# Kernel optimization log

Hardware: AMD Instinct MI355X
Metric: run time of the kernel (lower is better)

Reference implementation:

```python
import jax, jax.numpy as jnp
import numpy as np

# Module config (from init_kwargs)
B = 1024          # batch
CIN = 1024        # in_channels
COUT = 2048       # out_channels
K = 7             # kernel_size; input spatial must equal K so deform-conv out is 1x1
STRIDE, PAD, DIL, DG = 1, 0, 1, 1  # stride, padding, dilation, deformable_groups
H = W = K


def setup_inputs() -> dict:
    key = jax.random.key(0)
    k1, k2, k3, k4, k5, k6 = jax.random.split(key, 6)
    x = jax.random.normal(k1, (B, CIN, H, W), dtype=jnp.float32)
    # offset-predicting conv: Conv2d(CIN, 2*K*K*DG, K, bias=False); small init so offsets are a few pixels
    offset_w = jax.random.normal(k2, (2 * DG * K * K, CIN, K, K), dtype=jnp.float32) * 0.01
    # deformable conv weight/bias (kaiming-like scale)
    deform_w = jax.random.normal(k3, (COUT, CIN, K, K), dtype=jnp.float32) * (1.0 / np.sqrt(CIN * K * K))
    deform_b = jax.random.normal(k4, (COUT,), dtype=jnp.float32) * 0.01
    # fused linear COUT -> COUT
    lin_w = jax.random.normal(k5, (COUT, COUT), dtype=jnp.float32) * (1.0 / np.sqrt(COUT))
    lin_b = jax.random.normal(k6, (COUT,), dtype=jnp.float32) * 0.01
    return {"x": x, "offset_w": offset_w, "deform_w": deform_w,
            "deform_b": deform_b, "lin_w": lin_w, "lin_b": lin_b}


def _deform_conv2d(x, offset, weight, bias):
    """torchvision deform_conv2d (v1, no modulation mask), groups=1.
    x: [B, C, H, W]; offset: [B, 2*DG*K*K, Ho, Wo] ordered (dg, kh, kw, (dy,dx)).
    """
    Bn, C, Hx, Wx = x.shape
    Cout, _, Kh, Kw = weight.shape
    P = Kh * Kw
    Ho, Wo = offset.shape[2], offset.shape[3]
    L = Ho * Wo
    Cg = C // DG

    off = offset.reshape(Bn, DG, P, 2, Ho, Wo)
    ky = jnp.repeat(jnp.arange(Kh), Kw).astype(x.dtype)   # [P]
    kx = jnp.tile(jnp.arange(Kw), Kh).astype(x.dtype)     # [P]
    base_y = (jnp.arange(Ho) * STRIDE - PAD).astype(x.dtype)  # [Ho]
    base_x = (jnp.arange(Wo) * STRIDE - PAD).astype(x.dtype)  # [Wo]
    # sampling positions [B, DG, P, Ho, Wo]
    py = off[:, :, :, 0] + (ky * DIL)[None, None, :, None, None] + base_y[None, None, None, :, None]
    px = off[:, :, :, 1] + (kx * DIL)[None, None, :, None, None] + base_x[None, None, None, None, :]

    y0 = jnp.floor(py); x0 = jnp.floor(px)
    fy = py - y0;       fx = px - x0
    y0i = y0.astype(jnp.int32); x0i = x0.astype(jnp.int32)

    xg = x.reshape(Bn, DG, Cg, Hx * Wx)
    acc = jnp.zeros((Bn, DG, Cg, P * L), x.dtype)
    for di, wy in ((0, 1.0 - fy), (1, fy)):
        for dj, wx in ((0, 1.0 - fx), (1, fx)):
            yi = y0i + di
            xi = x0i + dj
            valid = (yi >= 0) & (yi < Hx) & (xi >= 0) & (xi < Wx)  # zero-pad outside
            idx = (jnp.clip(yi, 0, Hx - 1) * Wx + jnp.clip(xi, 0, Wx - 1)).reshape(Bn, DG, 1, P * L)
            wgt = (wy * wx * valid.astype(x.dtype)).reshape(Bn, DG, 1, P * L)
            g = jnp.take_along_axis(xg, jnp.broadcast_to(idx, (Bn, DG, Cg, P * L)), axis=-1)
            acc = acc + g * wgt
    # columns: [B, C*P, L] with (channel, kernel-tap) ordering matching weight layout
    cols = acc.reshape(Bn, DG, Cg, P, L).reshape(Bn, C * P, L)
    out = jnp.einsum('ok,bkl->bol', weight.reshape(Cout, C * P), cols) + bias[None, :, None]
    return out.reshape(Bn, Cout, Ho, Wo)


def reference(x, offset_w, deform_w, deform_b, lin_w, lin_b):
    # 1) offset-predicting conv (bias=False)
    offset = jax.lax.conv_general_dilated(
        x, offset_w, window_strides=(STRIDE, STRIDE),
        padding=[(PAD, PAD), (PAD, PAD)], rhs_dilation=(DIL, DIL),
        dimension_numbers=('NCHW', 'OIHW', 'NCHW'))  # [B, 2*DG*K*K, 1, 1]
    # 2) deformable conv
    y = _deform_conv2d(x, offset, deform_w, deform_b)  # [B, COUT, 1, 1]
    # 3) linear over flattened features (spatial is 1x1 so flat dim == COUT)
    y = y.reshape(B, COUT) @ lin_w.T + lin_b
    # 4) softshrink(lambd=0.5)
    y = jnp.where(y > 0.5, y - 0.5, jnp.where(y < -0.5, y + 0.5, jnp.zeros_like(y)))
    return y.reshape(B, COUT, 1, 1)
```

## Files before the change

### kernel.cpp

```cpp
#include <hip/hip_runtime.h>

typedef _Float16 f16;
typedef _Float16 f16x8 __attribute__((ext_vector_type(8)));
typedef float f32x4 __attribute__((ext_vector_type(4)));

#define DEVI static __device__ __forceinline__

DEVI void async_ld16(const void* g, void* l) {
  __builtin_amdgcn_global_load_lds(
      (const __attribute__((address_space(1))) unsigned int*)g,
      (__attribute__((address_space(3))) unsigned int*)l, 16, 0, 0);
}

DEVI int sw_off(int row, int q) {
  return row * 64 + ((q ^ ((row >> 1) & 3)) << 4);
}

template<bool A_F32>
__global__ __launch_bounds__(256, 2)
void gemm_bt(const void* __restrict__ Aptr, const f16* __restrict__ Bt,
             float* __restrict__ Cpart, int ldK, int Nvalid,
             int mTiles, int nTiles, int kPerSplit, int Mtot) {
  __shared__ __align__(16) f16 As[128 * 32];
  __shared__ __align__(16) f16 Bs[128 * 32];

  int nb = gridDim.x;
  int bid = (blockIdx.x & 7) * (nb >> 3) + (blockIdx.x >> 3);
  int ms = bid % mTiles; bid /= mTiles;
  int ns = bid % nTiles; bid /= nTiles;
  int ks = bid;
  int m0 = ms * 128, n0 = ns * 128;
  int k0 = ks * kPerSplit;

  int tid = threadIdx.x;
  int w = tid >> 6, lane = tid & 63;
  int wrow = (w >> 1) * 64, wcol = (w & 1) * 64;
  int lrow = lane & 15, lquad = lane >> 4;

  f32x4 acc[4][4];
#pragma unroll
  for (int i = 0; i < 4; ++i)
#pragma unroll
    for (int j = 0; j < 4; ++j) acc[i][j] = (f32x4){0.f, 0.f, 0.f, 0.f};

  for (int kk = k0; kk < k0 + kPerSplit; kk += 32) {
    __syncthreads();
#pragma unroll
    for (int s = 0; s < 2; ++s) {
      int rl = w * 32 + s * 16 + (lane >> 2);
      int qp = lane & 3;
      int q = qp ^ ((rl >> 1) & 3);
      int rb = n0 + rl; if (rb > Nvalid - 1) rb = Nvalid - 1;
      async_ld16(Bt + (size_t)rb * ldK + kk + q * 8, &Bs[(w * 32 + s * 16) * 32]);
    }
    if (!A_F32) {
      const f16* Ah = (const f16*)Aptr;
#pragma unroll
      for (int s = 0; s < 2; ++s) {
        int rl = w * 32 + s * 16 + (lane >> 2);
        int qp = lane & 3;
        int q = qp ^ ((rl >> 1) & 3);
        async_ld16(Ah + (size_t)(m0 + rl) * ldK + kk + q * 8, &As[(w * 32 + s * 16) * 32]);
      }
    } else {
      const float* Af = (const float*)Aptr;
      int r = tid >> 1, half = tid & 1;
      const float* src = Af + (size_t)(m0 + r) * ldK + kk + half * 16;
      float v[16];
#pragma unroll
      for (int u = 0; u < 4; ++u) {
        f32x4 t4 = *(const f32x4*)(src + u * 4);
        v[u * 4 + 0] = t4[0]; v[u * 4 + 1] = t4[1];
        v[u * 4 + 2] = t4[2]; v[u * 4 + 3] = t4[3];
      }
#pragma unroll
      for (int u2 = 0; u2 < 2; ++u2) {
        f16x8 h;
#pragma unroll
        for (int e = 0; e < 8; ++e) h[e] = (f16)v[u2 * 8 + e];
        *(f16x8*)((char*)As + sw_off(r, half * 2 + u2)) = h;
      }
    }
    __syncthreads();

    f16x8 af[4], bf[4];
#pragma unroll
    for (int i = 0; i < 4; ++i)
      af[i] = *(const f16x8*)((const char*)As + sw_off(wrow + i * 16 + lrow, lquad));
#pragma unroll
    for (int j = 0; j < 4; ++j)
      bf[j] = *(const f16x8*)((const char*)Bs + sw_off(wcol + j * 16 + lrow, lquad));
#pragma unroll
    for (int i = 0; i < 4; ++i)
#pragma unroll
      for (int j = 0; j < 4; ++j)
        acc[i][j] = __builtin_amdgcn_mfma_f32_16x16x32_f16(af[i], bf[j], acc[i][j], 0, 0, 0);
  }

  size_t base = (size_t)ks * Mtot * Nvalid;
#pragma unroll
  for (int i = 0; i < 4; ++i) {
    int row = m0 + wrow + i * 16 + lquad * 4;
#pragma unroll
    for (int j = 0; j < 4; ++j) {
      int col = n0 + wcol + j * 16 + lrow;
      if (col < Nvalid) {
#pragma unroll
        for (int r = 0; r < 4; ++r)
          Cpart[base + (size_t)(row + r) * Nvalid + col] = acc[i][j][r];
      }
    }
  }
}

__global__ void cvt_f32_to_f16(const float* __restrict__ in, f16* __restrict__ out, long n) {
  long idx = ((long)blockIdx.x * blockDim.x + threadIdx.x) * 8;
  if (idx + 8 <= n) {
    f32x4 a = *(const f32x4*)(in + idx);
    f32x4 b = *(const f32x4*)(in + idx + 4);
    f16x8 o;
    o[0] = (f16)a[0]; o[1] = (f16)a[1]; o[2] = (f16)a[2]; o[3] = (f16)a[3];
    o[4] = (f16)b[0]; o[5] = (f16)b[1]; o[6] = (f16)b[2]; o[7] = (f16)b[3];
    *(f16x8*)(out + idx) = o;
  }
}

__global__ __launch_bounds__(256)
void build_cols(const float* __restrict__ x, const float* __restrict__ offs,
                f16* __restrict__ cols) {
  int b = blockIdx.x;
  __shared__ int s_idx[49][4];
  __shared__ float s_w[49][4];
  int t = threadIdx.x;
  if (t < 49) {
    float dy = offs[b * 98 + 2 * t];
    float dx = offs[b * 98 + 2 * t + 1];
    float py = dy + (float)(t / 7);
    float px = dx + (float)(t % 7);
    float fy0 = floorf(py), fx0 = floorf(px);
    int y0 = (int)fy0, x0 = (int)fx0;
    float fy = py - fy0, fx = px - fx0;
#pragma unroll
    for (int di = 0; di < 2; ++di)
#pragma unroll
      for (int dj = 0; dj < 2; ++dj) {
        int yi = y0 + di, xi = x0 + dj;
        bool valid = (yi >= 0) && (yi < 7) && (xi >= 0) && (xi < 7);
        int yc = yi < 0 ? 0 : (yi > 6 ? 6 : yi);
        int xc = xi < 0 ? 0 : (xi > 6 ? 6 : xi);
        float wy = di ? fy : 1.f - fy;
        float wx = dj ? fx : 1.f - fx;
        s_idx[t][di * 2 + dj] = yc * 7 + xc;
        s_w[t][di * 2 + dj] = valid ? wy * wx : 0.f;
      }
  }
  __syncthreads();
  const float* xb = x + (size_t)b * 50176;
  f16* cb = cols + (size_t)b * 50176;
  for (int k0 = t * 8; k0 < 50176; k0 += 256 * 8) {
    f16x8 h;
#pragma unroll
    for (int u = 0; u < 8; ++u) {
      int k = k0 + u;
      int c = k / 49;
      int p = k - c * 49;
      const float* xc = xb + c * 49;
      float v = s_w[p][0] * xc[s_idx[p][0]] + s_w[p][1] * xc[s_idx[p][1]]
              + s_w[p][2] * xc[s_idx[p][2]] + s_w[p][3] * xc[s_idx[p][3]];
      h[u] = (f16)v;
    }
    *(f16x8*)(cb + k0) = h;
  }
}

__global__ void combine_k(const float* __restrict__ parts, int nparts, size_t pstride,
                          const float* __restrict__ bias, float* __restrict__ outf,
                          f16* __restrict__ outh, int total, int cols, int shrink) {
  int i = blockIdx.x * 256 + threadIdx.x;
  if (i >= total) return;
  float s = 0.f;
  for (int p = 0; p < nparts; ++p) s += parts[(size_t)p * pstride + i];
  if (bias) s += bias[i % cols];
  if (shrink) s = s > 0.5f ? s - 0.5f : (s < -0.5f ? s + 0.5f : 0.f);
  if (outf) outf[i] = s;
  if (outh) outh[i] = (f16)s;
}

extern "C" void kernel_launch(void* const* d_in, const int* in_sizes, int n_in,
                              void* d_out, int out_size, void* d_ws, size_t ws_size,
                              hipStream_t stream) {
  const float* x  = (const float*)d_in[0];
  const float* ow = (const float*)d_in[1];
  const float* dw = (const float*)d_in[2];
  const float* db = (const float*)d_in[3];
  const float* lw = (const float*)d_in[4];
  const float* lb = (const float*)d_in[5];
  float* out = (float*)d_out;

  const long KX = 50176;
  char* ws = (char*)d_ws;
  size_t off = 0;
  auto alloc = [&](size_t bytes) {
    char* p = ws + off;
    off = (off + bytes + 255) & ~(size_t)255;
    return p;
  };
  f16*   dw_h = (f16*)  alloc((size_t)2048 * KX * 2);
  f16*   ow_h = (f16*)  alloc((size_t)98 * KX * 2);
  f16*   lw_h = (f16*)  alloc((size_t)2048 * 2048 * 2);
  float* offp = (float*)alloc((size_t)32 * 1024 * 98 * 4);
  float* offs = (float*)alloc((size_t)1024 * 98 * 4);
  f16*   cols = (f16*)  alloc((size_t)1024 * KX * 2);
  float* y1p  = (float*)alloc((size_t)4 * 1024 * 2048 * 4);
  f16*   y1h  = (f16*)  alloc((size_t)1024 * 2048 * 2);
  float* y2p  = (float*)alloc((size_t)2 * 1024 * 2048 * 4);
  if (off > ws_size) return;

  long n_dw = 2048L * KX, n_ow = 98L * KX, n_lw = 2048L * 2048L;
  cvt_f32_to_f16<<<(unsigned)(n_dw / 8 / 256), 256, 0, stream>>>(dw, dw_h, n_dw);
  cvt_f32_to_f16<<<(unsigned)(n_ow / 8 / 256), 256, 0, stream>>>(ow, ow_h, n_ow);
  cvt_f32_to_f16<<<(unsigned)(n_lw / 8 / 256), 256, 0, stream>>>(lw, lw_h, n_lw);

  gemm_bt<true><<<8 * 1 * 32, 256, 0, stream>>>(x, ow_h, offp, 50176, 98, 8, 1, 1568, 1024);
  combine_k<<<(1024 * 98 + 255) / 256, 256, 0, stream>>>(
      offp, 32, (size_t)1024 * 98, nullptr, offs, nullptr, 1024 * 98, 98, 0);

  build_cols<<<1024, 256, 0, stream>>>(x, offs, cols);

  gemm_bt<false><<<8 * 16 * 4, 256, 0, stream>>>(cols, dw_h, y1p, 50176, 2048, 8, 16, 12544, 1024);
  combine_k<<<(2097152 + 255) / 256, 256, 0, stream>>>(
      y1p, 4, (size_t)2097152, db, nullptr, y1h, 2097152, 2048, 0);

  gemm_bt<false><<<8 * 16 * 2, 256, 0, stream>>>(y1h, lw_h, y2p, 2048, 2048, 8, 16, 1024, 1024);
  combine_k<<<(2097152 + 255) / 256, 256, 0, stream>>>(
      y2p, 2, (size_t)2097152, lb, out, nullptr, 2097152, 2048, 1);
}
```

Baseline: 1.263 ms.

## Raise split-K parallelism, stage x in LDS for column build, reuse workspace

Increases split-K factors for all three GEMMs (more blocks, smaller K slices) and raises launch-bounds occupancy to 4 blocks per SM. The column builder is split into 8 blocks per batch that first stage a 128-channel slice of x in shared memory and gather from there, instead of reading scattered global addresses. Workspace buffers are aliased (offsets inside y1p, y2p reusing cols) to fit the larger partial buffers. The trade-off is more partial-sum traffic in the combine kernels and possible register spilling under the tighter occupancy bound.

```diff
diff --git a/kernel.cpp b/kernel.cpp
--- a/kernel.cpp
+++ b/kernel.cpp
@@ -17,7 +17,7 @@
 }
 
 template<bool A_F32>
-__global__ __launch_bounds__(256, 2)
+__global__ __launch_bounds__(256, 4)
 void gemm_bt(const void* __restrict__ Aptr, const f16* __restrict__ Bt,
              float* __restrict__ Cpart, int ldK, int Nvalid,
              int mTiles, int nTiles, int kPerSplit, int Mtot) {
@@ -66,18 +66,13 @@
       const float* Af = (const float*)Aptr;
       int r = tid >> 1, half = tid & 1;
       const float* src = Af + (size_t)(m0 + r) * ldK + kk + half * 16;
-      float v[16];
-#pragma unroll
-      for (int u = 0; u < 4; ++u) {
-        f32x4 t4 = *(const f32x4*)(src + u * 4);
-        v[u * 4 + 0] = t4[0]; v[u * 4 + 1] = t4[1];
-        v[u * 4 + 2] = t4[2]; v[u * 4 + 3] = t4[3];
-      }
 #pragma unroll
       for (int u2 = 0; u2 < 2; ++u2) {
+        f32x4 a = *(const f32x4*)(src + u2 * 8);
+        f32x4 b = *(const f32x4*)(src + u2 * 8 + 4);
         f16x8 h;
-#pragma unroll
-        for (int e = 0; e < 8; ++e) h[e] = (f16)v[u2 * 8 + e];
+        h[0] = (f16)a[0]; h[1] = (f16)a[1]; h[2] = (f16)a[2]; h[3] = (f16)a[3];
+        h[4] = (f16)b[0]; h[5] = (f16)b[1]; h[6] = (f16)b[2]; h[7] = (f16)b[3];
         *(f16x8*)((char*)As + sw_off(r, half * 2 + u2)) = h;
       }
     }
@@ -125,12 +120,14 @@
   }
 }
 
-__global__ __launch_bounds__(256)
+__global__ __launch_bounds__(256, 4)
 void build_cols(const float* __restrict__ x, const float* __restrict__ offs,
                 f16* __restrict__ cols) {
-  int b = blockIdx.x;
-  __shared__ int s_idx[49][4];
-  __shared__ float s_w[49][4];
+  int b = blockIdx.x >> 3;
+  int c0 = (blockIdx.x & 7) * 128;
+  __shared__ __align__(16) float s_x[128 * 49];
+  __shared__ __align__(16) int   s_idx[49][4];
+  __shared__ __align__(16) float s_w[49][4];
   int t = threadIdx.x;
   if (t < 49) {
     float dy = offs[b * 98 + 2 * t];
@@ -154,22 +151,27 @@
         s_w[t][di * 2 + dj] = valid ? wy * wx : 0.f;
       }
   }
+  const f32x4* xs = (const f32x4*)(x + (size_t)b * 50176 + c0 * 49);
+  f32x4* s4 = (f32x4*)s_x;
+#pragma unroll
+  for (int i = 0; i < 6; ++i) s4[t + i * 256] = xs[t + i * 256];
+  if (t < 32) s4[1536 + t] = xs[1536 + t];
   __syncthreads();
-  const float* xb = x + (size_t)b * 50176;
-  f16* cb = cols + (size_t)b * 50176;
-  for (int k0 = t * 8; k0 < 50176; k0 += 256 * 8) {
-    f16x8 h;
-#pragma unroll
-    for (int u = 0; u < 8; ++u) {
-      int k = k0 + u;
-      int c = k / 49;
-      int p = k - c * 49;
-      const float* xc = xb + c * 49;
-      float v = s_w[p][0] * xc[s_idx[p][0]] + s_w[p][1] * xc[s_idx[p][1]]
-              + s_w[p][2] * xc[s_idx[p][2]] + s_w[p][3] * xc[s_idx[p][3]];
-      h[u] = (f16)v;
-    }
-    *(f16x8*)(cb + k0) = h;
+
+  f16* cb = cols + (size_t)b * 50176 + c0 * 49;
+#pragma unroll
+  for (int i = 0; i < 25; ++i) {
+    int o = t + i * 256;
+    if (o < 6272) {
+      unsigned c = (unsigned)o / 49u;
+      unsigned p = (unsigned)o - c * 49u;
+      int4  gi = *(const int4*)s_idx[p];
+      float4 gw = *(const float4*)s_w[p];
+      const float* row = s_x + c * 49;
+      float v = gw.x * row[gi.x] + gw.y * row[gi.y]
+              + gw.z * row[gi.z] + gw.w * row[gi.w];
+      cb[o] = (f16)v;
+    }
   }
 }
 
@@ -208,12 +210,12 @@
   f16*   dw_h = (f16*)  alloc((size_t)2048 * KX * 2);
   f16*   ow_h = (f16*)  alloc((size_t)98 * KX * 2);
   f16*   lw_h = (f16*)  alloc((size_t)2048 * 2048 * 2);
-  float* offp = (float*)alloc((size_t)32 * 1024 * 98 * 4);
-  float* offs = (float*)alloc((size_t)1024 * 98 * 4);
   f16*   cols = (f16*)  alloc((size_t)1024 * KX * 2);
-  float* y1p  = (float*)alloc((size_t)4 * 1024 * 2048 * 4);
+  float* y1p  = (float*)alloc((size_t)8 * 1024 * 2048 * 4);
   f16*   y1h  = (f16*)  alloc((size_t)1024 * 2048 * 2);
-  float* y2p  = (float*)alloc((size_t)2 * 1024 * 2048 * 4);
+  float* offs = (float*)y1p;
+  float* offp = (float*)((char*)y1p + (1u << 20));
+  float* y2p  = (float*)cols;
   if (off > ws_size) return;
 
   long n_dw = 2048L * KX, n_ow = 98L * KX, n_lw = 2048L * 2048L;
@@ -221,17 +223,20 @@
   cvt_f32_to_f16<<<(unsigned)(n_ow / 8 / 256), 256, 0, stream>>>(ow, ow_h, n_ow);
   cvt_f32_to_f16<<<(unsigned)(n_lw / 8 / 256), 256, 0, stream>>>(lw, lw_h, n_lw);
 
-  gemm_bt<true><<<8 * 1 * 32, 256, 0, stream>>>(x, ow_h, offp, 50176, 98, 8, 1, 1568, 1024);
+  gemm_bt<true><<<8 * 1 * 98, 256, 0, stream>>>(
+      x, ow_h, offp, 50176, 98, 8, 1, 512, 1024);
   combine_k<<<(1024 * 98 + 255) / 256, 256, 0, stream>>>(
-      offp, 32, (size_t)1024 * 98, nullptr, offs, nullptr, 1024 * 98, 98, 0);
-
-  build_cols<<<1024, 256, 0, stream>>>(x, offs, cols);
-
-  gemm_bt<false><<<8 * 16 * 4, 256, 0, stream>>>(cols, dw_h, y1p, 50176, 2048, 8, 16, 12544, 1024);
+      offp, 98, (size_t)1024 * 98, nullptr, offs, nullptr, 1024 * 98, 98, 0);
+
+  build_cols<<<1024 * 8, 256, 0, stream>>>(x, offs, cols);
+
+  gemm_bt<false><<<8 * 16 * 8, 256, 0, stream>>>(
+      cols, dw_h, y1p, 50176, 2048, 8, 16, 6272, 1024);
   combine_k<<<(2097152 + 255) / 256, 256, 0, stream>>>(
-      y1p, 4, (size_t)2097152, db, nullptr, y1h, 2097152, 2048, 0);
-
-  gemm_bt<false><<<8 * 16 * 2, 256, 0, stream>>>(y1h, lw_h, y2p, 2048, 2048, 8, 16, 1024, 1024);
+      y1p, 8, (size_t)2097152, db, nullptr, y1h, 2097152, 2048, 0);
+
+  gemm_bt<false><<<8 * 16 * 8, 256, 0, stream>>>(
+      y1h, lw_h, y2p, 2048, 2048, 8, 16, 256, 1024);
   combine_k<<<(2097152 + 255) / 256, 256, 0, stream>>>(
-      y2p, 2, (size_t)2097152, lb, out, nullptr, 2097152, 2048, 1);
-}
+      y2p, 8, (size_t)2097152, lb, out, nullptr, 2097152, 2048, 1);
+}
```

New measurement: 1.111 ms. 1.14x faster.
